# Optimization experiments

Hardware: AMD Instinct MI355X
Metric: run time of the kernel (lower is better)

The kernel has to match this reference:

```python
import jax, jax.numpy as jnp
import numpy as np

NEG_SLOPE = 0.01  # nn.LeakyReLU default


def conv3x3(x, w, b):
    # x: [B,C,H,W], w: [O,I,3,3], stride 1, pad 1
    y = jax.lax.conv_general_dilated(x, w, (1, 1), 'SAME',
                                     dimension_numbers=('NCHW', 'OIHW', 'NCHW'))
    return y + b[None, :, None, None]


def bilinear_gather(img, ys, xs):
    # img: [B,C,H,W]; ys, xs: [B,K,H,W] float sample coords -> [B,C,K,H,W]
    B, C, H, W = img.shape
    imgf = img.reshape(B, C, H * W)
    y0 = jnp.floor(ys)
    x0 = jnp.floor(xs)
    out = jnp.zeros((B, C) + ys.shape[1:], img.dtype)
    for dy in (0, 1):
        for dx in (0, 1):
            yc = y0 + dy
            xc = x0 + dx
            wgt = (1.0 - jnp.abs(ys - yc)) * (1.0 - jnp.abs(xs - xc))
            valid = (yc >= 0) & (yc <= H - 1) & (xc >= 0) & (xc <= W - 1)
            wgt = jnp.where(valid, wgt, 0.0)
            idx = (jnp.clip(yc, 0, H - 1) * W + jnp.clip(xc, 0, W - 1)).astype(jnp.int32)
            g = jax.vmap(lambda f, i: f[:, i])(imgf, idx)  # [B,C,K,H,W]
            out = out + wgt[:, None] * g
    return out


def dcn_v2(x, off_feat, w_off, b_off, w, b):
    # Modulated deformable 3x3 conv (DCNv2Pack, extra_offset_mask=True, dg=1).
    B, C, H, W = x.shape
    om = conv3x3(off_feat, w_off, b_off)            # [B, 27, H, W]
    o1, o2, m = jnp.split(om, 3, axis=1)            # each [B, 9, H, W]
    off = jnp.concatenate([o1, o2], axis=1)         # [B, 18, H, W]
    off_y = off[:, 0::2]                            # [B, 9, H, W]
    off_x = off[:, 1::2]
    mask = jax.nn.sigmoid(m)                        # [B, 9, H, W]
    k = jnp.arange(3, dtype=x.dtype) - 1.0
    ky = jnp.repeat(k, 3)                           # row-major kernel order
    kx = jnp.tile(k, 3)
    hh = jnp.arange(H, dtype=x.dtype)[:, None]
    ww = jnp.arange(W, dtype=x.dtype)[None, :]
    ys = hh[None, None] + ky[None, :, None, None] + off_y
    xs = ww[None, None] + kx[None, :, None, None] + off_x
    sampled = bilinear_gather(x, ys, xs)            # [B,C,9,H,W]
    wk = w.reshape(w.shape[0], C, 9)
    out = jnp.einsum('oik,bkhw,bikhw->bohw', wk, mask, sampled)
    return out + b[None, :, None, None]


def setup_inputs() -> dict:
    key = jax.random.key(0)
    ks = jax.random.split(key, 12)
    B, C, OC, H, W = 4, 64, 32, 128, 128
    s = 0.02
    return {
        'input': jax.random.normal(ks[0], (B, C, H, W), jnp.float32),
        'offset': jax.random.normal(ks[1], (B, OC, H, W), jnp.float32),
        'w_off1': jax.random.normal(ks[2], (27, OC, 3, 3), jnp.float32) * s,
        'b_off1': jnp.zeros((27,), jnp.float32),
        'w1': jax.random.normal(ks[3], (C, C, 3, 3), jnp.float32) * s,
        'b1': jnp.zeros((C,), jnp.float32),
        'w_off2': jax.random.normal(ks[4], (27, OC, 3, 3), jnp.float32) * s,
        'b_off2': jnp.zeros((27,), jnp.float32),
        'w2': jax.random.normal(ks[5], (C, C, 3, 3), jnp.float32) * s,
        'b2': jnp.zeros((C,), jnp.float32),
        'w_last': jax.random.normal(ks[6], (C, C, 3, 3), jnp.float32) * s,
        'b_last': jnp.zeros((C,), jnp.float32),
    }


def reference(input, offset, w_off1, b_off1, w1, b1,
              w_off2, b_off2, w2, b2, w_last, b_last):
    x = dcn_v2(input, offset, w_off1, b_off1, w1, b1)
    x = jnp.where(x >= 0, x, NEG_SLOPE * x)
    out = dcn_v2(x, offset, w_off2, b_off2, w2, b2) + input
    return conv3x3(out, w_last, b_last)
```

## Files before the change

kernel.cpp:

```cpp
#include <hip/hip_runtime.h>
#include <cmath>

#define HW   16384
#define Wd   128
#define Hd   128
#define NB   4

typedef __attribute__((ext_vector_type(8))) _Float16 h16x8;
typedef __attribute__((ext_vector_type(4))) float f32x4;
typedef __attribute__((ext_vector_type(4))) unsigned int u32x4;

__device__ inline unsigned short f2h(float f) {
    _Float16 h = (_Float16)f;
    return __builtin_bit_cast(unsigned short, h);
}
__device__ inline float h2f(unsigned short u) {
    return (float)__builtin_bit_cast(_Float16, u);
}
__device__ inline _Float16 u2h(unsigned short u) {
    return __builtin_bit_cast(_Float16, u);
}

__device__ inline void repack_one(int idx, const float* __restrict__ s1, const float* __restrict__ s2,
                                  int Osplit, int O, int CIN, int KS, unsigned short* __restrict__ dst) {
    int e    = idx & 7;
    int lane = (idx >> 3) & 63;
    int ks   = (idx >> 9) % KS;
    int m    = (idx / (512 * KS)) & 3;
    int k    = idx / (2048 * KS);
    int oc = m * 16 + (lane & 15);
    int c  = ks * 32 + (lane >> 4) * 8 + e;
    float v = 0.f;
    if (oc < O && c < CIN)
        v = (oc < Osplit) ? s1[((size_t)oc * CIN + c) * 9 + k]
                          : s2[((size_t)(oc - Osplit) * CIN + c) * 9 + k];
    dst[idx] = f2h(v);
}

__global__ __launch_bounds__(256) void prep(
    const float* __restrict__ input, const float* __restrict__ offset,
    const float* __restrict__ w_off1, const float* __restrict__ w_off2,
    const float* __restrict__ b_off1, const float* __restrict__ b_off2,
    const float* __restrict__ w1, const float* __restrict__ w2, const float* __restrict__ w_last,
    unsigned short* __restrict__ xn, unsigned short* __restrict__ offn,
    unsigned short* __restrict__ wfo, unsigned short* __restrict__ wf1,
    unsigned short* __restrict__ wf2, unsigned short* __restrict__ wfl,
    float* __restrict__ bias54)
{
    int blk = blockIdx.x;
    if (blk < 512) {
        int t = blk * 256 + threadIdx.x;
        if (t < 65536) {
            int b = t >> 14, p = t & 16383;
            const float* s = input + ((size_t)b * 64) * HW + p;
            unsigned short* d = xn + (size_t)t * 64;
#pragma unroll
            for (int g = 0; g < 8; g++) {
                unsigned short pk[8];
#pragma unroll
                for (int e = 0; e < 8; e++) pk[e] = f2h(s[(size_t)(g * 8 + e) * HW]);
                *(u32x4*)(d + g * 8) = *(u32x4*)pk;
            }
        } else {
            int u = t - 65536;
            int b = u >> 14, p = u & 16383;
            const float* s = offset + ((size_t)b * 32) * HW + p;
            unsigned short* d = offn + (size_t)u * 32;
#pragma unroll
            for (int g = 0; g < 4; g++) {
                unsigned short pk[8];
#pragma unroll
                for (int e = 0; e < 8; e++) pk[e] = f2h(s[(size_t)(g * 8 + e) * HW]);
                *(u32x4*)(d + g * 8) = *(u32x4*)pk;
            }
        }
    } else {
        int u = (blk - 512) * 256 + threadIdx.x;
        if (u < 18432)        repack_one(u, w_off1, w_off2, 27, 54, 32, 1, wfo);
        else if (u < 55296)   repack_one(u - 18432, w1, w1, 64, 64, 64, 2, wf1);
        else if (u < 92160)   repack_one(u - 55296, w2, w2, 64, 64, 64, 2, wf2);
        else if (u < 129024)  repack_one(u - 92160, w_last, w_last, 64, 64, 64, 2, wfl);
        else if (u < 129078) {
            int j = u - 129024;
            bias54[j] = (j < 27) ? b_off1[j] : b_off2[j - 27];
        }
    }
}

__global__ __launch_bounds__(256, 4) void conv_stage32(
    const unsigned short* __restrict__ xn, const unsigned short* __restrict__ wf,
    const float* __restrict__ bias, unsigned short* __restrict__ out)
{
    __shared__ __align__(16) unsigned short stage[198 * 32];
    int lb = ((blockIdx.x & 7) << 7) | (blockIdx.x >> 3);
    int t = threadIdx.x;
    int pxbase = lb * 64;
    int b = pxbase >> 14;
    int pbase = pxbase & 16383;
    int rowbase = pbase >> 7, colbase = pbase & 127;
    const unsigned short* xb = xn + ((size_t)(b << 14)) * 32;

    for (int q = t; q < 792; q += 256) {
        int ps = q >> 2, j = q & 3;
        int ly = ps / 66, lx = ps - ly * 66;
        int y = rowbase - 1 + ly, x = colbase - 1 + lx;
        bool ok = (y >= 0) & (y < Hd) & (x >= 0) & (x < Wd);
        u32x4 v = {0, 0, 0, 0};
        if (ok) v = *(const u32x4*)(xb + ((size_t)(y * Wd + x)) * 32 + j * 8);
        *(u32x4*)(stage + ps * 32 + ((j ^ (ps & 3)) << 3)) = v;
    }
    __syncthreads();

    int lane = t & 63, wv = t >> 6;
    int sp = wv * 16 + (lane & 15);
    int px = pxbase + sp;
    int p = px & 16383;
    int cg = lane >> 4;

    const h16x8* wfv = (const h16x8*)wf;
    f32x4 acc[4];
#pragma unroll
    for (int m = 0; m < 4; m++) acc[m] = (f32x4){0.f, 0.f, 0.f, 0.f};

#pragma unroll
    for (int k = 0; k < 9; k++) {
        int ps = (k / 3) * 66 + sp + (k % 3);
        h16x8 bq = *(const h16x8*)(stage + ps * 32 + ((cg ^ (ps & 3)) << 3));
        h16x8 aF[4];
#pragma unroll
        for (int m = 0; m < 4; m++)
            aF[m] = wfv[(k * 4 + m) * 64 + lane];
#pragma unroll
        for (int m = 0; m < 4; m++)
            acc[m] = __builtin_amdgcn_mfma_f32_16x16x32_f16(aF[m], bq, acc[m], 0, 0, 0);
    }

#pragma unroll
    for (int m = 0; m < 4; m++) {
        int ocb = m * 16 + cg * 4;
#pragma unroll
        for (int r = 0; r < 4; r++) {
            int oc = ocb + r;
            if (oc < 54)
                out[((size_t)b * 54 + oc) * HW + p] = f2h(acc[m][r] + bias[oc]);
        }
    }
}

__global__ __launch_bounds__(512, 8) void conv_stage64(
    const unsigned short* __restrict__ xn, const unsigned short* __restrict__ wf,
    const float* __restrict__ bias, float* __restrict__ out)
{
    __shared__ __align__(16) unsigned short stage[198 * 64];
    int lb = ((blockIdx.x & 7) << 7) | (blockIdx.x >> 3);
    int t = threadIdx.x;
    int pxbase = lb * 64;
    int b = pxbase >> 14;
    int pbase = pxbase & 16383;
    int rowbase = pbase >> 7, colbase = pbase & 127;
    const unsigned short* xb = xn + ((size_t)(b << 14)) * 64;

    for (int q = t; q < 1584; q += 512) {
        int ps = q >> 3, j = q & 7;
        int ly = ps / 66, lx = ps - ly * 66;
        int y = rowbase - 1 + ly, x = colbase - 1 + lx;
        bool ok = (y >= 0) & (y < Hd) & (x >= 0) & (x < Wd);
        u32x4 v = {0, 0, 0, 0};
        if (ok) v = *(const u32x4*)(xb + ((size_t)(y * Wd + x)) * 64 + j * 8);
        *(u32x4*)(stage + ps * 64 + ((j ^ (ps & 7)) << 3)) = v;
    }
    __syncthreads();

    int lane = t & 63;
    int wave = t >> 6;
    int kh = wave >> 2;
    int wv = wave & 3;
    int sp = wv * 16 + (lane & 15);
    int px = pxbase + sp;
    int p = px & 16383;
    int cg = lane >> 4;
    int cch = kh * 4 + cg;

    const h16x8* wfv = (const h16x8*)wf;
    f32x4 acc[4];
#pragma unroll
    for (int m = 0; m < 4; m++) acc[m] = (f32x4){0.f, 0.f, 0.f, 0.f};

#pragma unroll
    for (int k = 0; k < 9; k++) {
        int ps = (k / 3) * 66 + sp + (k % 3);
        h16x8 bq = *(const h16x8*)(stage + ps * 64 + ((cch ^ (ps & 7)) << 3));
        h16x8 aF[4];
#pragma unroll
        for (int m = 0; m < 4; m++)
            aF[m] = wfv[((k * 4 + m) * 2 + kh) * 64 + lane];
#pragma unroll
        for (int m = 0; m < 4; m++)
            acc[m] = __builtin_amdgcn_mfma_f32_16x16x32_f16(aF[m], bq, acc[m], 0, 0, 0);
    }

    __syncthreads();
    float* red = (float*)stage;
    if (kh == 1) {
#pragma unroll
        for (int m = 0; m < 4; m++)
#pragma unroll
            for (int j = 0; j < 4; j++)
                red[(m * 4 + j) * 256 + wv * 64 + lane] = acc[m][j];
    }
    __syncthreads();
    if (kh == 0) {
#pragma unroll
        for (int m = 0; m < 4; m++) {
            int ocb = m * 16 + cg * 4;
#pragma unroll
            for (int r = 0; r < 4; r++) {
                int oc = ocb + r;
                float v = acc[m][r] + red[(m * 4 + r) * 256 + wv * 64 + lane] + bias[oc];
                out[((size_t)b * 64 + oc) * HW + p] = v;
            }
        }
    }
}

struct Tap { float w00, w01, w10, w11; int o00, o01, o10, o11; };

__device__ inline Tap mkparams(float oy, float ox, float mv, int row, int col, int k) {
    Tap P;
    float mk = 1.f / (1.f + __expf(-mv));
    float ys = (float)(row + k / 3 - 1) + oy;
    float xs = (float)(col + k % 3 - 1) + ox;
    float y0f = floorf(ys), x0f = floorf(xs);
    float fy = ys - y0f, fx = xs - x0f;
    int y0 = (int)y0f, x0 = (int)x0f;
    int y1 = y0 + 1, x1 = x0 + 1;
    bool vy0 = (y0 >= 0) & (y0 < Hd);
    bool vy1 = (y1 >= 0) & (y1 < Hd);
    bool vx0 = (x0 >= 0) & (x0 < Wd);
    bool vx1 = (x1 >= 0) & (x1 < Wd);
    P.w00 = (vy0 && vx0) ? (1.f - fy) * (1.f - fx) * mk : 0.f;
    P.w01 = (vy0 && vx1) ? (1.f - fy) * fx * mk : 0.f;
    P.w10 = (vy1 && vx0) ? fy * (1.f - fx) * mk : 0.f;
    P.w11 = (vy1 && vx1) ? fy * fx * mk : 0.f;
    int iy0 = min(max(y0, 0), Hd - 1) * Wd;
    int iy1 = min(max(y1, 0), Hd - 1) * Wd;
    int ix0 = min(max(x0, 0), Wd - 1);
    int ix1 = min(max(x1, 0), Wd - 1);
    P.o00 = iy0 + ix0; P.o01 = iy0 + ix1; P.o10 = iy1 + ix0; P.o11 = iy1 + ix1;
    return P;
}

template<int EPI>
__global__ __launch_bounds__(512, 4) void dcn_stage(
    const unsigned short* __restrict__ xn, const unsigned short* __restrict__ omh, int omOff,
    const unsigned short* __restrict__ wf, const float* __restrict__ bias,
    const float* __restrict__ resid, unsigned short* __restrict__ outn)
{
    __shared__ __align__(16) unsigned short stage[490 * 64];
    __shared__ unsigned twp0[576], twp1[576];
    __shared__ unsigned tap0[576], tap1[576];
    __shared__ unsigned short tof[4][576];

    int lb = ((blockIdx.x & 7) << 7) | (blockIdx.x >> 3);
    int t = threadIdx.x;
    int pxbase = lb * 64;
    int b = pxbase >> 14;
    int pbase = pxbase & 16383;
    int rowbase = pbase >> 7;
    int colbase = pbase & 127;
    int ybase = rowbase - 3;
    int xbase = colbase - 3;
    const unsigned short* xb = xn + ((size_t)(b << 14)) * 64;

    for (int s = t; s < 576; s += 512) {
        int k = s >> 6, sp = s & 63;
        int p = pbase + sp;
        int row = p >> 7, col = p & 127;
        const unsigned short* omb = omh + ((size_t)b * 54 + omOff) * HW + p;
        float oy = h2f(omb[(size_t)(2 * k) * HW]);
        float ox = h2f(omb[(size_t)(2 * k + 1) * HW]);
        float mv = h2f(omb[(size_t)(18 + k) * HW]);
        Tap P = mkparams(oy, ox, mv, row, col, k);

        unsigned a[4];
        int oo[4] = {P.o00, P.o01, P.o10, P.o11};
#pragma unroll
        for (int c = 0; c < 4; c++) {
            int o = oo[c];
            int y = o >> 7, x = o & 127;
            int ly = y - ybase, lx = x - xbase;
            bool inw = ((unsigned)ly < 7u) & ((unsigned)lx < 70u);
            int ps = min(max(ly, 0), 6) * 70 + min(max(lx, 0), 69);
            a[c] = (inw ? 0u : 0x8000u) | (unsigned)((ps << 3) | (ps & 7));
            tof[c][s] = (unsigned short)o;
        }
        twp0[s] = (unsigned)f2h(P.w00) | ((unsigned)f2h(P.w01) << 16);
        twp1[s] = (unsigned)f2h(P.w10) | ((unsigned)f2h(P.w11) << 16);
        tap0[s] = a[0] | (a[1] << 16);
        tap1[s] = a[2] | (a[3] << 16);
    }
    for (int q = t; q < 3920; q += 512) {
        int ps = q >> 3, j = q & 7;
        int ly = ps / 70, lx = ps - ly * 70;
        int y = min(max(ybase + ly, 0), Hd - 1);
        int x = min(max(xbase + lx, 0), Wd - 1);
        u32x4 v = *(const u32x4*)(xb + ((size_t)(y * Wd + x)) * 64 + j * 8);
        *(u32x4*)(stage + ps * 64 + ((j ^ (ps & 7)) << 3)) = v;
    }
    __syncthreads();

    int lane = t & 63;
    int wave = t >> 6;
    int kh = wave >> 2;
    int wv = wave & 3;
    int sp = wv * 16 + (lane & 15);
    int px = pxbase + sp;
    int p = px & 16383;
    int cg = lane >> 4;
    int c0 = kh * 32 + cg * 8;
    int cch = kh * 4 + cg;

    const h16x8* wfv = (const h16x8*)wf;

    f32x4 acc[4];
#pragma unroll
    for (int m = 0; m < 4; m++) acc[m] = (f32x4){0.f, 0.f, 0.f, 0.f};

#pragma unroll
    for (int k = 0; k < 9; k++) {
        int s = k * 64 + sp;
        unsigned a01 = tap0[s], a23 = tap1[s];
        unsigned w01 = twp0[s], w23 = twp1[s];

        unsigned code[4] = { a01 & 0x7fffu, (a01 >> 16) & 0x7fffu,
                             a23 & 0x7fffu, (a23 >> 16) & 0x7fffu };
        h16x8 gc[4];
#pragma unroll
        for (int c = 0; c < 4; c++)
            gc[c] = *(const h16x8*)((const char*)stage + ((code[c] ^ (unsigned)cch) << 4));

        if (__builtin_expect((a01 | a23) & 0x80008000u, 0)) {
            unsigned fb[4] = { a01 & 0x8000u, a01 & 0x80000000u,
                               a23 & 0x8000u, a23 & 0x80000000u };
#pragma unroll
            for (int c = 0; c < 4; c++)
                if (fb[c])
                    gc[c] = *(const h16x8*)(xb + (size_t)tof[c][s] * 64 + c0);
        }

        _Float16 h00 = u2h((unsigned short)(w01 & 0xffffu));
        _Float16 h01 = u2h((unsigned short)(w01 >> 16));
        _Float16 h10 = u2h((unsigned short)(w23 & 0xffffu));
        _Float16 h11 = u2h((unsigned short)(w23 >> 16));
        h16x8 bF = gc[0] * h00;
        bF = gc[1] * h01 + bF;
        bF = gc[2] * h10 + bF;
        bF = gc[3] * h11 + bF;

        h16x8 aF[4];
#pragma unroll
        for (int m = 0; m < 4; m++)
            aF[m] = wfv[((k * 4 + m) * 2 + kh) * 64 + lane];
#pragma unroll
        for (int m = 0; m < 4; m++)
            acc[m] = __builtin_amdgcn_mfma_f32_16x16x32_f16(aF[m], bF, acc[m], 0, 0, 0);
    }

    __syncthreads();
    float* red = (float*)stage;
    if (kh == 1) {
#pragma unroll
        for (int m = 0; m < 4; m++)
#pragma unroll
            for (int j = 0; j < 4; j++)
                red[(m * 4 + j) * 256 + wv * 64 + lane] = acc[m][j];
    }
    __syncthreads();
    if (kh == 0) {
        unsigned short* drow = outn + (size_t)px * 64;
#pragma unroll
        for (int m = 0; m < 4; m++) {
            int ocb = m * 16 + cg * 4;
            unsigned short pk[4];
#pragma unroll
            for (int r = 0; r < 4; r++) {
                int oc = ocb + r;
                float v = acc[m][r] + red[(m * 4 + r) * 256 + wv * 64 + lane] + bias[oc];
                if (EPI == 0) v = (v >= 0.f) ? v : 0.01f * v;
                if (EPI == 1) v += resid[((size_t)b * 64 + oc) * HW + p];
                pk[r] = f2h(v);
            }
            *(ushort4*)(drow + ocb) = *(ushort4*)pk;
        }
    }
}

extern "C" void kernel_launch(void* const* d_in, const int* in_sizes, int n_in,
                              void* d_out, int out_size, void* d_ws, size_t ws_size,
                              hipStream_t stream)
{
    const float* input  = (const float*)d_in[0];
    const float* offset = (const float*)d_in[1];
    const float* w_off1 = (const float*)d_in[2];
    const float* b_off1 = (const float*)d_in[3];
    const float* w1     = (const float*)d_in[4];
    const float* b1     = (const float*)d_in[5];
    const float* w_off2 = (const float*)d_in[6];
    const float* b_off2 = (const float*)d_in[7];
    const float* w2     = (const float*)d_in[8];
    const float* b2     = (const float*)d_in[9];
    const float* w_last = (const float*)d_in[10];
    const float* b_last = (const float*)d_in[11];
    float* out = (float*)d_out;

    float* ws = (float*)d_ws;
    unsigned short* omh = (unsigned short*)ws;
    unsigned short* xn   = (unsigned short*)(ws + 3538944);
    unsigned short* offn = xn + 4194304;
    unsigned short* x1n  = offn + 2097152;
    unsigned short* x2n  = x1n + 4194304;
    unsigned short* wfo  = x2n + 4194304;
    unsigned short* wf1  = wfo + 18432;
    unsigned short* wf2  = wf1 + 36864;
    unsigned short* wfl  = wf2 + 36864;
    float* bias54 = (float*)(wfl + 36864);

    prep<<<dim3(1018), 256, 0, stream>>>(input, offset, w_off1, w_off2, b_off1, b_off2,
                                         w1, w2, w_last, xn, offn, wfo, wf1, wf2, wfl, bias54);

    conv_stage32<<<dim3(1024), 256, 0, stream>>>(offn, wfo, bias54, omh);
    dcn_stage<0><<<dim3(1024), 512, 0, stream>>>(xn, omh, 0, wf1, b1, nullptr, x1n);
    dcn_stage<1><<<dim3(1024), 512, 0, stream>>>(x1n, omh, 27, wf2, b2, input, x2n);
    conv_stage64<<<dim3(1024), 512, 0, stream>>>(x2n, wfl, b_last, out);
}
```

Before: 81.15 us.

## Fuse offset/mask conv into each DCN stage kernel, dropping separate offset-conv launch

```diff
diff --git a/kernel.cpp b/kernel.cpp
--- a/kernel.cpp
+++ b/kernel.cpp
@@ -13,9 +13,6 @@
 __device__ inline unsigned short f2h(float f) {
     _Float16 h = (_Float16)f;
     return __builtin_bit_cast(unsigned short, h);
-}
-__device__ inline float h2f(unsigned short u) {
-    return (float)__builtin_bit_cast(_Float16, u);
 }
 __device__ inline _Float16 u2h(unsigned short u) {
     return __builtin_bit_cast(_Float16, u);
@@ -76,73 +73,14 @@
         }
     } else {
         int u = (blk - 512) * 256 + threadIdx.x;
-        if (u < 18432)        repack_one(u, w_off1, w_off2, 27, 54, 32, 1, wfo);
-        else if (u < 55296)   repack_one(u - 18432, w1, w1, 64, 64, 64, 2, wf1);
-        else if (u < 92160)   repack_one(u - 55296, w2, w2, 64, 64, 64, 2, wf2);
-        else if (u < 129024)  repack_one(u - 92160, w_last, w_last, 64, 64, 64, 2, wfl);
-        else if (u < 129078) {
-            int j = u - 129024;
+        if (u < 18432)        repack_one(u, w_off1, w_off1, 27, 27, 32, 1, wfo);
+        else if (u < 36864)   repack_one(u - 18432, w_off2, w_off2, 27, 27, 32, 1, wfo + 18432);
+        else if (u < 73728)   repack_one(u - 36864, w1, w1, 64, 64, 64, 2, wf1);
+        else if (u < 110592)  repack_one(u - 73728, w2, w2, 64, 64, 64, 2, wf2);
+        else if (u < 147456)  repack_one(u - 110592, w_last, w_last, 64, 64, 64, 2, wfl);
+        else if (u < 147510) {
+            int j = u - 147456;
             bias54[j] = (j < 27) ? b_off1[j] : b_off2[j - 27];
-        }
-    }
-}
-
-__global__ __launch_bounds__(256, 4) void conv_stage32(
-    const unsigned short* __restrict__ xn, const unsigned short* __restrict__ wf,
-    const float* __restrict__ bias, unsigned short* __restrict__ out)
-{
-    __shared__ __align__(16) unsigned short stage[198 * 32];
-    int lb = ((blockIdx.x & 7) << 7) | (blockIdx.x >> 3);
-    int t = threadIdx.x;
-    int pxbase = lb * 64;
-    int b = pxbase >> 14;
-    int pbase = pxbase & 16383;
-    int rowbase = pbase >> 7, colbase = pbase & 127;
-    const unsigned short* xb = xn + ((size_t)(b << 14)) * 32;
-
-    for (int q = t; q < 792; q += 256) {
-        int ps = q >> 2, j = q & 3;
-        int ly = ps / 66, lx = ps - ly * 66;
-        int y = rowbase - 1 + ly, x = colbase - 1 + lx;
-        bool ok = (y >= 0) & (y < Hd) & (x >= 0) & (x < Wd);
-        u32x4 v = {0, 0, 0, 0};
-        if (ok) v = *(const u32x4*)(xb + ((size_t)(y * Wd + x)) * 32 + j * 8);
-        *(u32x4*)(stage + ps * 32 + ((j ^ (ps & 3)) << 3)) = v;
-    }
-    __syncthreads();
-
-    int lane = t & 63, wv = t >> 6;
-    int sp = wv * 16 + (lane & 15);
-    int px = pxbase + sp;
-    int p = px & 16383;
-    int cg = lane >> 4;
-
-    const h16x8* wfv = (const h16x8*)wf;
-    f32x4 acc[4];
-#pragma unroll
-    for (int m = 0; m < 4; m++) acc[m] = (f32x4){0.f, 0.f, 0.f, 0.f};
-
-#pragma unroll
-    for (int k = 0; k < 9; k++) {
-        int ps = (k / 3) * 66 + sp + (k % 3);
-        h16x8 bq = *(const h16x8*)(stage + ps * 32 + ((cg ^ (ps & 3)) << 3));
-        h16x8 aF[4];
-#pragma unroll
-        for (int m = 0; m < 4; m++)
-            aF[m] = wfv[(k * 4 + m) * 64 + lane];
-#pragma unroll
-        for (int m = 0; m < 4; m++)
-            acc[m] = __builtin_amdgcn_mfma_f32_16x16x32_f16(aF[m], bq, acc[m], 0, 0, 0);
-    }
-
-#pragma unroll
-    for (int m = 0; m < 4; m++) {
-        int ocb = m * 16 + cg * 4;
-#pragma unroll
-        for (int r = 0; r < 4; r++) {
-            int oc = ocb + r;
-            if (oc < 54)
-                out[((size_t)b * 54 + oc) * HW + p] = f2h(acc[m][r] + bias[oc]);
         }
     }
 }
@@ -251,15 +189,18 @@
 }
 
 template<int EPI>
-__global__ __launch_bounds__(512, 4) void dcn_stage(
-    const unsigned short* __restrict__ xn, const unsigned short* __restrict__ omh, int omOff,
+__global__ __launch_bounds__(512, 4) void dcn_fused(
+    const unsigned short* __restrict__ xn, const unsigned short* __restrict__ offn,
+    const unsigned short* __restrict__ wfo, const float* __restrict__ obias,
     const unsigned short* __restrict__ wf, const float* __restrict__ bias,
     const float* __restrict__ resid, unsigned short* __restrict__ outn)
 {
     __shared__ __align__(16) unsigned short stage[490 * 64];
     __shared__ unsigned twp0[576], twp1[576];
     __shared__ unsigned tap0[576], tap1[576];
-    __shared__ unsigned short tof[4][576];
+
+    unsigned short* offstage = stage;
+    float* omt = (float*)(stage + 6336);
 
     int lb = ((blockIdx.x & 7) << 7) | (blockIdx.x >> 3);
     int t = threadIdx.x;
@@ -271,15 +212,57 @@
     int ybase = rowbase - 3;
     int xbase = colbase - 3;
     const unsigned short* xb = xn + ((size_t)(b << 14)) * 64;
+    const unsigned short* ob = offn + ((size_t)(b << 14)) * 32;
+
+    for (int q = t; q < 792; q += 512) {
+        int ps = q >> 2, j = q & 3;
+        int ly = ps / 66, lx = ps - ly * 66;
+        int y = rowbase - 1 + ly, x = colbase - 1 + lx;
+        bool ok = (y >= 0) & (y < Hd) & (x >= 0) & (x < Wd);
+        u32x4 v = {0, 0, 0, 0};
+        if (ok) v = *(const u32x4*)(ob + ((size_t)(y * Wd + x)) * 32 + j * 8);
+        *(u32x4*)(offstage + ps * 32 + ((j ^ (ps & 3)) << 3)) = v;
+    }
+    __syncthreads();
+
+    int lane = t & 63;
+    int wave = t >> 6;
+
+    if (wave < 4) {
+        int osp = wave * 16 + (lane & 15);
+        int cg4 = lane >> 4;
+        const h16x8* wfv = (const h16x8*)wfo;
+        f32x4 oacc[2];
+#pragma unroll
+        for (int m = 0; m < 2; m++) oacc[m] = (f32x4){0.f, 0.f, 0.f, 0.f};
+#pragma unroll
+        for (int k = 0; k < 9; k++) {
+            int ps = (k / 3) * 66 + osp + (k % 3);
+            h16x8 bq = *(const h16x8*)(offstage + ps * 32 + ((cg4 ^ (ps & 3)) << 3));
+#pragma unroll
+            for (int m = 0; m < 2; m++) {
+                h16x8 aF = wfv[(k * 4 + m) * 64 + lane];
+                oacc[m] = __builtin_amdgcn_mfma_f32_16x16x32_f16(aF, bq, oacc[m], 0, 0, 0);
+            }
+        }
+#pragma unroll
+        for (int m = 0; m < 2; m++) {
+            int ocb = m * 16 + cg4 * 4;
+#pragma unroll
+            for (int r = 0; r < 4; r++) {
+                int oc = ocb + r;
+                if (oc < 27) omt[oc * 64 + osp] = oacc[m][r] + obias[oc];
+            }
+        }
+    }
+    __syncthreads();
 
     for (int s = t; s < 576; s += 512) {
-        int k = s >> 6, sp = s & 63;
-        int p = pbase + sp;
-        int row = p >> 7, col = p & 127;
-        const unsigned short* omb = omh + ((size_t)b * 54 + omOff) * HW + p;
-        float oy = h2f(omb[(size_t)(2 * k) * HW]);
-        float ox = h2f(omb[(size_t)(2 * k + 1) * HW]);
-        float mv = h2f(omb[(size_t)(18 + k) * HW]);
+        int k = s >> 6, sp2 = s & 63;
+        int row = rowbase, col = colbase + sp2;
+        float oy = omt[(2 * k) * 64 + sp2];
+        float ox = omt[(2 * k + 1) * 64 + sp2];
+        float mv = omt[(18 + k) * 64 + sp2];
         Tap P = mkparams(oy, ox, mv, row, col, k);
 
         unsigned a[4];
@@ -291,14 +274,15 @@
             int ly = y - ybase, lx = x - xbase;
             bool inw = ((unsigned)ly < 7u) & ((unsigned)lx < 70u);
             int ps = min(max(ly, 0), 6) * 70 + min(max(lx, 0), 69);
-            a[c] = (inw ? 0u : 0x8000u) | (unsigned)((ps << 3) | (ps & 7));
-            tof[c][s] = (unsigned short)o;
+            a[c] = inw ? (unsigned)((ps << 3) | (ps & 7)) : (0x8000u | (unsigned)o);
         }
         twp0[s] = (unsigned)f2h(P.w00) | ((unsigned)f2h(P.w01) << 16);
         twp1[s] = (unsigned)f2h(P.w10) | ((unsigned)f2h(P.w11) << 16);
         tap0[s] = a[0] | (a[1] << 16);
         tap1[s] = a[2] | (a[3] << 16);
     }
+    __syncthreads();
+
     for (int q = t; q < 3920; q += 512) {
         int ps = q >> 3, j = q & 7;
         int ly = ps / 70, lx = ps - ly * 70;
@@ -309,8 +293,6 @@
     }
     __syncthreads();
 
-    int lane = t & 63;
-    int wave = t >> 6;
     int kh = wave >> 2;
     int wv = wave & 3;
     int sp = wv * 16 + (lane & 15);
@@ -332,20 +314,17 @@
         unsigned a01 = tap0[s], a23 = tap1[s];
         unsigned w01 = twp0[s], w23 = twp1[s];
 
-        unsigned code[4] = { a01 & 0x7fffu, (a01 >> 16) & 0x7fffu,
-                             a23 & 0x7fffu, (a23 >> 16) & 0x7fffu };
+        unsigned code[4] = { a01 & 0xffffu, a01 >> 16, a23 & 0xffffu, a23 >> 16 };
         h16x8 gc[4];
 #pragma unroll
         for (int c = 0; c < 4; c++)
-            gc[c] = *(const h16x8*)((const char*)stage + ((code[c] ^ (unsigned)cch) << 4));
+            gc[c] = *(const h16x8*)((const char*)stage + (((code[c] & 0xFFFu) ^ (unsigned)cch) << 4));
 
         if (__builtin_expect((a01 | a23) & 0x80008000u, 0)) {
-            unsigned fb[4] = { a01 & 0x8000u, a01 & 0x80000000u,
-                               a23 & 0x8000u, a23 & 0x80000000u };
 #pragma unroll
             for (int c = 0; c < 4; c++)
-                if (fb[c])
-                    gc[c] = *(const h16x8*)(xb + (size_t)tof[c][s] * 64 + c0);
+                if (code[c] & 0x8000u)
+                    gc[c] = *(const h16x8*)(xb + (size_t)(code[c] & 0x7fffu) * 64 + c0);
         }
 
         _Float16 h00 = u2h((unsigned short)(w01 & 0xffffu));
@@ -413,23 +392,22 @@
     const float* b_last = (const float*)d_in[11];
     float* out = (float*)d_out;
 
-    float* ws = (float*)d_ws;
-    unsigned short* omh = (unsigned short*)ws;
-    unsigned short* xn   = (unsigned short*)(ws + 3538944);
+    unsigned short* xn   = (unsigned short*)d_ws;
     unsigned short* offn = xn + 4194304;
     unsigned short* x1n  = offn + 2097152;
     unsigned short* x2n  = x1n + 4194304;
     unsigned short* wfo  = x2n + 4194304;
-    unsigned short* wf1  = wfo + 18432;
+    unsigned short* wf1  = wfo + 36864;
     unsigned short* wf2  = wf1 + 36864;
     unsigned short* wfl  = wf2 + 36864;
     float* bias54 = (float*)(wfl + 36864);
 
-    prep<<<dim3(1018), 256, 0, stream>>>(input, offset, w_off1, w_off2, b_off1, b_off2,
+    prep<<<dim3(1089), 256, 0, stream>>>(input, offset, w_off1, w_off2, b_off1, b_off2,
                                          w1, w2, w_last, xn, offn, wfo, wf1, wf2, wfl, bias54);
 
-    conv_stage32<<<dim3(1024), 256, 0, stream>>>(offn, wfo, bias54, omh);
-    dcn_stage<0><<<dim3(1024), 512, 0, stream>>>(xn, omh, 0, wf1, b1, nullptr, x1n);
-    dcn_stage<1><<<dim3(1024), 512, 0, stream>>>(x1n, omh, 27, wf2, b2, input, x2n);
+    dcn_fused<0><<<dim3(1024), 512, 0, stream>>>(xn, offn, wfo, bias54,
+                                                 wf1, b1, nullptr, x1n);
+    dcn_fused<1><<<dim3(1024), 512, 0, stream>>>(x1n, offn, wfo + 18432, bias54 + 27,
+                                                 wf2, b2, input, x2n);
     conv_stage64<<<dim3(1024), 512, 0, stream>>>(x2n, wfl, b_last, out);
 }
```

New measurement: 79.39 us. 2.2% less time.
